# Kernel tuning notes

Hardware: AMD Instinct MI355X
Metric: run time of the kernel (lower is better)

## Reference

```python
import jax, jax.numpy as jnp
import numpy as np

D_MODEL = 1024
NHEAD = 16
D_K = D_MODEL // NHEAD  # 64
B, L = 2, 2048


def _apply_rotary(x, cos, sin):
    # x: (B, H, L, d_k); cos/sin: (B, L, d_k//2)
    d_half = x.shape[-1] // 2
    x1, x2 = x[..., :d_half], x[..., d_half:]
    c = cos[:, None, :, :]
    s = sin[:, None, :, :]
    return jnp.concatenate([x1 * c - x2 * s, x1 * s + x2 * c], axis=-1)


def setup_inputs() -> dict:
    key = jax.random.key(0)
    ks = jax.random.split(key, 7)
    x = jax.random.normal(ks[0], (B, L, D_MODEL), dtype=jnp.float32)
    rope_cos = jax.random.uniform(ks[1], (B, L, D_K // 2), dtype=jnp.float32)
    rope_sin = jax.random.uniform(ks[2], (B, L, D_K // 2), dtype=jnp.float32)
    # Linear params (PyTorch layout: weight (out, in), y = x @ W.T + b)
    lim_qkv = 1.0 / np.sqrt(D_MODEL)
    W_qkv = jax.random.uniform(ks[3], (3 * D_MODEL, D_MODEL), dtype=jnp.float32, minval=-lim_qkv, maxval=lim_qkv)
    b_qkv = jax.random.uniform(ks[4], (3 * D_MODEL,), dtype=jnp.float32, minval=-lim_qkv, maxval=lim_qkv)
    W_out = jax.random.uniform(ks[5], (D_MODEL, D_MODEL), dtype=jnp.float32, minval=-lim_qkv, maxval=lim_qkv)
    b_out = jax.random.uniform(ks[6], (D_MODEL,), dtype=jnp.float32, minval=-lim_qkv, maxval=lim_qkv)
    return {"x": x, "rope_cos": rope_cos, "rope_sin": rope_sin,
            "W_qkv": W_qkv, "b_qkv": b_qkv, "W_out": W_out, "b_out": b_out}


def reference(x, rope_cos, rope_sin, W_qkv, b_qkv, W_out, b_out):
    Bx, Lx, D = x.shape
    scale = D_K ** -0.5
    qkv = x @ W_qkv.T + b_qkv                     # (B, L, 3D)
    qkv = qkv.reshape(Bx, Lx, 3, NHEAD, D_K)
    q = jnp.transpose(qkv[:, :, 0], (0, 2, 1, 3))  # (B, H, L, d_k)
    k = jnp.transpose(qkv[:, :, 1], (0, 2, 1, 3))
    v = jnp.transpose(qkv[:, :, 2], (0, 2, 1, 3))
    q = _apply_rotary(q, rope_cos, rope_sin)
    k = _apply_rotary(k, rope_cos, rope_sin)
    attn = jnp.einsum("bhqd,bhkd->bhqk", q, k) * scale  # (B, H, L, L)
    attn = jax.nn.softmax(attn, axis=-1)
    out = jnp.einsum("bhqk,bhkd->bhqd", attn, v)          # (B, H, L, d_k)
    out = jnp.transpose(out, (0, 2, 1, 3)).reshape(Bx, Lx, D)
    return out @ W_out.T + b_out
```

## Files before the change

kernel.cpp:

```cpp
#include <hip/hip_runtime.h>
#include <hip/hip_bf16.h>
#include <stdint.h>


typedef __attribute__((ext_vector_type(8)))  short bf16x8;
typedef __attribute__((ext_vector_type(4)))  float f32x4;
typedef __attribute__((ext_vector_type(16))) float f32x16;
typedef __attribute__((ext_vector_type(4)))  short short4v;
typedef __attribute__((ext_vector_type(4)))  unsigned int u32x4;

#define DEV static __device__ __forceinline__

DEV short f2bf(float f) {
  uint32_t u = __builtin_bit_cast(uint32_t, f);
  u += 0x7FFFu + ((u >> 16) & 1u);
  return (short)(u >> 16);
}
DEV float bf2f(short s) {
  return __builtin_bit_cast(float, ((uint32_t)(uint16_t)s) << 16);
}
DEV uint32_t pkbf(float a, float b) {
  __hip_bfloat162 h = __float22bfloat162_rn(make_float2(a, b));
  uint32_t u;
  __builtin_memcpy(&u, &h, 4);
  return u;
}
DEV void pl32swap(uint32_t &dst, uint32_t &src) {
  asm volatile("v_permlane32_swap_b32 %0, %1" : "+v"(dst), "+v"(src));
}

#define AS1 __attribute__((address_space(1)))
#define AS3 __attribute__((address_space(3)))
#define GLOAD_LDS16(gp, lp) \
  __builtin_amdgcn_global_load_lds((const AS1 void*)(gp), (AS3 void*)(lp), 16, 0, 0)

__global__ void k_cvt_bf16(const float* __restrict__ in, short* __restrict__ out, int n4) {
  int i = blockIdx.x * 256 + threadIdx.x;
  if (i >= n4) return;
  float4 v = reinterpret_cast<const float4*>(in)[i];
  short4v o = { f2bf(v.x), f2bf(v.y), f2bf(v.z), f2bf(v.w) };
  reinterpret_cast<short4v*>(out)[i] = o;
}

DEV void gemm_stage(const short* Ag, const short* Bg, int K_,
                    short* AsD, short* BsD, int tid) {
  #pragma unroll
  for (int p = 0; p < 4; ++p) {
    int f = p * 256 + tid;
    int row = f >> 3;
    int sch = (f & 7) ^ (row & 7);
    GLOAD_LDS16(Ag + (size_t)row * K_ + sch * 8, AsD + f * 8);
    GLOAD_LDS16(Bg + (size_t)row * K_ + sch * 8, BsD + f * 8);
  }
}

#define GEMM_BODY(A_, Bt_, K_)                                              \
  __shared__ short Lds[4 * 128 * 64];    \
  const int tid = threadIdx.x;                                              \
  const int lane = tid & 63;                                                \
  const int wid  = tid >> 6;                                                \
  const int lq = lane & 15, lg = lane >> 4;                                 \
  const int wr = wid >> 1, wc = wid & 1;                                    \
  const int m0 = blockIdx.y * 128;                                          \
  const int n0 = blockIdx.x * 128;                                          \
  f32x4 acc[4][4];                                                          \
  _Pragma("unroll")                                                         \
  for (int i = 0; i < 4; ++i)                                               \
    _Pragma("unroll")                                                       \
    for (int j = 0; j < 4; ++j) acc[i][j] = (f32x4){0.f, 0.f, 0.f, 0.f};    \
  const int KT = (K_) >> 6;                                                 \
  gemm_stage((A_) + (size_t)m0 * (K_), (Bt_) + (size_t)n0 * (K_), (K_),     \
             Lds, Lds + 8192, tid);                                         \
  __syncthreads();                                                          \
  int gbuf = 0;                                                             \
  for (int kt = 0; kt < KT; ++kt) {                                         \
    if (kt + 1 < KT)                                                        \
      gemm_stage((A_)  + (size_t)m0 * (K_) + (kt + 1) * 64,                 \
                 (Bt_) + (size_t)n0 * (K_) + (kt + 1) * 64, (K_),           \
                 Lds + (gbuf ^ 1) * 16384,                                  \
                 Lds + (gbuf ^ 1) * 16384 + 8192, tid);                     \
    const short* As = Lds + gbuf * 16384;                                   \
    const short* Bs = As + 8192;                                            \
    _Pragma("unroll")                                                       \
    for (int kk = 0; kk < 2; ++kk) {                                        \
      bf16x8 af[4], bfr[4];                                                 \
      _Pragma("unroll")                                                     \
      for (int i = 0; i < 4; ++i)                                           \
        af[i]  = *reinterpret_cast<const bf16x8*>(                          \
            &As[(wr*64 + i*16 + lq) * 64 + (((kk*4 + lg) ^ (lq & 7)) * 8)]);\
      _Pragma("unroll")                                                     \
      for (int j = 0; j < 4; ++j)                                           \
        bfr[j] = *reinterpret_cast<const bf16x8*>(                          \
            &Bs[(wc*64 + j*16 + lq) * 64 + (((kk*4 + lg) ^ (lq & 7)) * 8)]);\
      _Pragma("unroll")                                                     \
      for (int i = 0; i < 4; ++i)                                           \
        _Pragma("unroll")                                                   \
        for (int j = 0; j < 4; ++j)                                         \
          acc[i][j] = __builtin_amdgcn_mfma_f32_16x16x32_bf16(              \
              af[i], bfr[j], acc[i][j], 0, 0, 0);                           \
    }                                                                       \
    __syncthreads();                                                        \
    gbuf ^= 1;                                                              \
  }

__global__ __launch_bounds__(256) void k_gemm_qkv(
    const short* __restrict__ A, const short* __restrict__ Bt,
    const float* __restrict__ bias,
    const float* __restrict__ cosb, const float* __restrict__ sinb,
    short* __restrict__ Qb, short* __restrict__ Kb, short* __restrict__ Vt)
{
  GEMM_BODY(A, Bt, 1024)

  short* Ep = Lds + wid * 4096;
  const int cglob = n0 + wc * 64;
  if (cglob < 2048) {
    const bool isq = (cglob < 1024);
    const float QS = isq ? 0.125f * 1.4426950408889634f : 1.0f;
    short* dst = isq ? Qb : Kb;
    const int h = (cglob & 1023) >> 6;
    const float b0 = bias[cglob + lq],      b2 = bias[cglob + 32 + lq];
    const float b1 = bias[cglob + 16 + lq], b3 = bias[cglob + 48 + lq];
    #pragma unroll
    for (int i = 0; i < 4; ++i) {
      #pragma unroll
      for (int r = 0; r < 4; ++r) {
        int lloc = i*16 + lg*4 + r;
        int rg = m0 + wr*64 + lloc;
        float c0 = cosb[(size_t)rg * 32 + lq];
        float s0 = sinb[(size_t)rg * 32 + lq];
        float c1 = cosb[(size_t)rg * 32 + 16 + lq];
        float s1 = sinb[(size_t)rg * 32 + 16 + lq];
        float x1 = acc[i][0][r] + b0, x2 = acc[i][2][r] + b2;
        Ep[lloc*64 + lq]      = f2bf((x1 * c0 - x2 * s0) * QS);
        Ep[lloc*64 + 32 + lq] = f2bf((x1 * s0 + x2 * c0) * QS);
        float y1 = acc[i][1][r] + b1, y2 = acc[i][3][r] + b3;
        Ep[lloc*64 + 16 + lq] = f2bf((y1 * c1 - y2 * s1) * QS);
        Ep[lloc*64 + 48 + lq] = f2bf((y1 * s1 + y2 * c1) * QS);
      }
    }
    #pragma unroll
    for (int p = 0; p < 8; ++p) {
      int f = p * 64 + lane;
      int lloc = f >> 3, d0 = (f & 7) * 8;
      int rg = m0 + wr*64 + lloc;
      int bi = rg >> 11, ll = rg & 2047;
      bf16x8 v = *reinterpret_cast<const bf16x8*>(&Ep[lloc*64 + d0]);
      *reinterpret_cast<bf16x8*>(
          &dst[((size_t)(bi * 16 + h) * 2048 + ll) * 64 + d0]) = v;
    }
  } else {
    const int h = (cglob - 2048) >> 6;
    #pragma unroll
    for (int i = 0; i < 4; ++i) {
      int lloc = i*16 + lg*4;
      #pragma unroll
      for (int j = 0; j < 4; ++j) {
        int d = j * 16 + lq;
        float bv = bias[cglob + d];
        short4v pk4 = { f2bf(acc[i][j][0] + bv), f2bf(acc[i][j][1] + bv),
                        f2bf(acc[i][j][2] + bv), f2bf(acc[i][j][3] + bv) };
        *reinterpret_cast<short4v*>(
            &Ep[d*64 + (lloc ^ ((d & 7) << 3))]) = pk4;
      }
    }
    #pragma unroll
    for (int p = 0; p < 8; ++p) {
      int f = p * 64 + lane;
      int d = f >> 3, lc = (f & 7) * 8;
      bf16x8 v = *reinterpret_cast<const bf16x8*>(&Ep[d*64 + lc]);
      int lreal = lc ^ ((d & 7) << 3);
      int rg = m0 + wr*64 + lreal;
      int bi = rg >> 11, ll = rg & 2047;
      *reinterpret_cast<bf16x8*>(
          &Vt[((size_t)(bi * 16 + h) * 64 + d) * 2048 + ll]) = v;
    }
  }
}

__global__ __launch_bounds__(256) void k_gemm_out(
    const short* __restrict__ A, const short* __restrict__ Bt,
    const float* __restrict__ bias, float* __restrict__ C)
{
  GEMM_BODY(A, Bt, 1024)
  const int N = 1024;
  #pragma unroll
  for (int i = 0; i < 4; ++i) {
    int rbase = m0 + wr*64 + i*16 + lg*4;
    #pragma unroll
    for (int j = 0; j < 4; ++j) {
      int col = n0 + wc*64 + j*16 + lq;
      float bv = bias[col];
      #pragma unroll
      for (int r = 0; r < 4; ++r)
        C[(size_t)(rbase + r) * N + col] = acc[i][j][r] + bv;
    }
  }
}

__global__ __launch_bounds__(256, 4) void k_attn(
    const short* __restrict__ Q, const short* __restrict__ Kb,
    const short* __restrict__ Vt,
    short* __restrict__ P0, short* __restrict__ P1,
    float* __restrict__ L0, float* __restrict__ L1)
{
  __shared__ short Ks[2][64 * 64];
  __shared__ short Vs[2][64 * 64];
  const int tid = threadIdx.x;
  const int lane = tid & 63;
  const int wid  = tid >> 6;
  const int Lq = lane & 31;
  const int h  = lane >> 5;
  const int bh = blockIdx.y;
  const int q0 = blockIdx.x * 128 + wid * 32;
  const int b = bh >> 4, hh = bh & 15;
  const int t0 = blockIdx.z * 16;
  short* Pp = blockIdx.z ? P1 : P0;
  float* Lp = blockIdx.z ? L1 : L0;

  const short* Qp = Q  + ((size_t)bh * 2048 + q0 + Lq) * 64;
  const short* Kp = Kb + (size_t)bh * 2048 * 64;
  const short* Vp = Vt + (size_t)bh * 64 * 2048;

  #define STAGE_KV(c, t) do {                                              \
    const short* Kg_ = Kp + (size_t)(t) * 64 * 64;                         \
    const short* Vg_ = Vp + (size_t)(t) * 64;                              \
    _Pragma("unroll")                                                      \
    for (int p_ = 0; p_ < 2; ++p_) {                                       \
      int f_ = p_ * 256 + tid;                                             \
      int row_ = f_ >> 3;                                                  \
      int sch_ = (f_ & 7) ^ (row_ & 7);                                    \
      GLOAD_LDS16(Kg_ + row_ * 64 + sch_ * 8,            &Ks[c][f_ * 8]);  \
      GLOAD_LDS16(Vg_ + (size_t)row_ * 2048 + sch_ * 8,  &Vs[c][f_ * 8]);  \
    }                                                                      \
  } while (0)

  bf16x8 qf[4];
  #pragma unroll
  for (int ks = 0; ks < 4; ++ks)
    qf[ks] = *reinterpret_cast<const bf16x8*>(Qp + ks * 16 + h * 8);

  f32x16 o[2];
  #pragma unroll
  for (int nd = 0; nd < 2; ++nd)
    #pragma unroll
    for (int r = 0; r < 16; ++r) o[nd][r] = 0.f;
  float la0 = 0.f, la1 = 0.f;

  STAGE_KV(0, t0);
  asm volatile("s_waitcnt vmcnt(0)" ::: "memory");
  __syncthreads();

  for (int kk2 = 0; kk2 < 16; ++kk2) {
    const int cur = kk2 & 1;
    if (kk2 < 15) STAGE_KV(cur ^ 1, t0 + kk2 + 1);

    #pragma unroll
    for (int mb = 0; mb < 2; ++mb) {
      f32x16 sm;
      #pragma unroll
      for (int r = 0; r < 16; ++r) sm[r] = 0.f;
      #pragma unroll
      for (int ks = 0; ks < 4; ++ks) {
        bf16x8 kf = *reinterpret_cast<const bf16x8*>(
            &Ks[cur][(mb*32 + Lq) * 64 + (((ks*2 + h) ^ (Lq & 7)) * 8)]);
        sm = __builtin_amdgcn_mfma_f32_32x32x16_bf16(kf, qf[ks], sm, 0, 0, 0);
      }
      #pragma unroll
      for (int half = 0; half < 2; ++half) {
        float e0 = __builtin_amdgcn_exp2f(sm[8*half + 0]);
        float e1 = __builtin_amdgcn_exp2f(sm[8*half + 1]);
        float e2 = __builtin_amdgcn_exp2f(sm[8*half + 2]);
        float e3 = __builtin_amdgcn_exp2f(sm[8*half + 3]);
        float e4 = __builtin_amdgcn_exp2f(sm[8*half + 4]);
        float e5 = __builtin_amdgcn_exp2f(sm[8*half + 5]);
        float e6 = __builtin_amdgcn_exp2f(sm[8*half + 6]);
        float e7 = __builtin_amdgcn_exp2f(sm[8*half + 7]);
        la0 += (e0 + e1) + (e4 + e5);
        la1 += (e2 + e3) + (e6 + e7);
        uint32_t w0 = pkbf(e0, e1), w1 = pkbf(e2, e3);
        uint32_t w2 = pkbf(e4, e5), w3 = pkbf(e6, e7);
        pl32swap(w0, w2);
        pl32swap(w1, w3);
        u32x4 paw = { w0, w1, w2, w3 };
        bf16x8 pa = __builtin_bit_cast(bf16x8, paw);
        const int ksl = mb * 2 + half;
        #pragma unroll
        for (int nd = 0; nd < 2; ++nd) {
          bf16x8 vf = *reinterpret_cast<const bf16x8*>(
              &Vs[cur][(nd*32 + Lq) * 64 + (((ksl*2 + h) ^ (Lq & 7)) * 8)]);
          o[nd] = __builtin_amdgcn_mfma_f32_32x32x16_bf16(pa, vf, o[nd], 0, 0, 0);
        }
      }
    }
    asm volatile("s_waitcnt vmcnt(0)" ::: "memory");
    __syncthreads();
  }

  float l_part = la0 + la1;
  l_part += __shfl_xor(l_part, 32, 64);
  if (h == 0) Lp[((size_t)bh << 11) + q0 + Lq] = l_part;
  #pragma unroll
  for (int r = 0; r < 16; ++r) {
    int qrow = (r & 3) + 8 * (r >> 2) + 4 * h;
    size_t rowb = ((size_t)b * 2048 + q0 + qrow) * 1024 + hh * 64;
    Pp[rowb + Lq]      = f2bf(o[0][r]);
    Pp[rowb + 32 + Lq] = f2bf(o[1][r]);
  }
  #undef STAGE_KV
}

__global__ void k_merge(const short* __restrict__ P0, const short* __restrict__ P1,
                        const float* __restrict__ L0, const float* __restrict__ L1,
                        short* __restrict__ AO)
{
  int idx = blockIdx.x * 256 + threadIdx.x;
  int rg = idx >> 7;
  int c0 = (idx & 127) * 8;
  int bh = ((rg >> 11) << 4) + (c0 >> 6);
  size_t lix = ((size_t)bh << 11) + (rg & 2047);
  float inv = 1.f / (L0[lix] + L1[lix]);
  size_t off = (size_t)rg * 1024 + c0;
  bf16x8 a = *reinterpret_cast<const bf16x8*>(&P0[off]);
  bf16x8 bv = *reinterpret_cast<const bf16x8*>(&P1[off]);
  bf16x8 r;
  #pragma unroll
  for (int j = 0; j < 8; ++j)
    r[j] = f2bf((bf2f(a[j]) + bf2f(bv[j])) * inv);
  *reinterpret_cast<bf16x8*>(&AO[off]) = r;
}

extern "C" void kernel_launch(void* const* d_in, const int* in_sizes, int n_in,
                              void* d_out, int out_size, void* d_ws, size_t ws_size,
                              hipStream_t stream) {
  (void)in_sizes; (void)n_in; (void)out_size; (void)ws_size;
  const float* x    = (const float*)d_in[0];
  const float* rc   = (const float*)d_in[1];
  const float* rs   = (const float*)d_in[2];
  const float* Wqkv = (const float*)d_in[3];
  const float* bqkv = (const float*)d_in[4];
  const float* Wout = (const float*)d_in[5];
  const float* bout = (const float*)d_in[6];
  float* out = (float*)d_out;

  char* ws = (char*)d_ws;
  short* xb  = (short*)(ws);
  short* wqb = (short*)(ws + 8388608);
  short* wob = (short*)(ws + 14680064);
  short* Qb  = (short*)(ws + 16777216);
  short* Kb  = (short*)(ws + 25165824);
  short* Vt  = (short*)(ws + 33554432);
  short* P0  = (short*)(ws + 41943040);
  short* P1  = (short*)(ws + 50331648);
  float* L0  = (float*)(ws + 58720256);
  float* L1  = (float*)(ws + 58982400);

  k_cvt_bf16<<<4096, 256, 0, stream>>>(x,    xb,  1048576);
  k_cvt_bf16<<<3072, 256, 0, stream>>>(Wqkv, wqb, 786432);
  k_cvt_bf16<<<1024, 256, 0, stream>>>(Wout, wob, 262144);
  k_gemm_qkv<<<dim3(24, 32), 256, 0, stream>>>(xb, wqb, bqkv, rc, rs, Qb, Kb, Vt);
  k_attn<<<dim3(16, 32, 2), 256, 0, stream>>>(Qb, Kb, Vt, P0, P1, L0, L1);
  k_merge<<<2048, 256, 0, stream>>>(P0, P1, L0, L1, P0);
  k_gemm_out<<<dim3(8, 32), 256, 0, stream>>>(P0, wob, bout, out);
}
```

Before: 120.0 us.

## Fuse split-KV merge into output GEMM, remap blocks across XCDs, prioritize MFMA

Removes the separate merge kernel. The output projection GEMM now loads both partial attention outputs and their softmax denominators itself, normalises them in registers and writes the A tile into LDS, while the weight tile keeps using direct global-to-LDS loads. This drops one launch and one round trip through HBM for the merged activation, but adds register-staged loads and a division per element to the GEMM's main loop. It also remaps block IDs in the GEMMs and attention so neighbouring tiles land on the same XCD for L2 reuse, and raises wave priority around the MFMA sections in attention.

Measured after the change: 128.4 us. +7.1%, slower.

```diff
diff --git a/kernel.cpp b/kernel.cpp
--- a/kernel.cpp
+++ b/kernel.cpp
@@ -61,8 +61,11 @@
   const int wid  = tid >> 6;                                                \
   const int lq = lane & 15, lg = lane >> 4;                                 \
   const int wr = wid >> 1, wc = wid & 1;                                    \
-  const int m0 = blockIdx.y * 128;                                          \
-  const int n0 = blockIdx.x * 128;                                          \
+  int lin_ = blockIdx.y * gridDim.x + blockIdx.x;                           \
+  const int q_ = (gridDim.x * gridDim.y) >> 3;                              \
+  lin_ = (lin_ & 7) * q_ + (lin_ >> 3);                                     \
+  const int m0 = (lin_ / gridDim.x) * 128;                                  \
+  const int n0 = (lin_ % gridDim.x) * 128;                                  \
   f32x4 acc[4][4];                                                          \
   _Pragma("unroll")                                                         \
   for (int i = 0; i < 4; ++i)                                               \
@@ -178,10 +181,109 @@
 }
 
 __global__ __launch_bounds__(256) void k_gemm_out(
-    const short* __restrict__ A, const short* __restrict__ Bt,
+    const short* __restrict__ P0, const short* __restrict__ P1,
+    const float* __restrict__ L0, const float* __restrict__ L1,
+    const short* __restrict__ Bt,
     const float* __restrict__ bias, float* __restrict__ C)
 {
-  GEMM_BODY(A, Bt, 1024)
+  __shared__ short Lds[4 * 128 * 64];
+  const int tid = threadIdx.x;
+  const int lane = tid & 63;
+  const int wid  = tid >> 6;
+  const int lq = lane & 15, lg = lane >> 4;
+  const int wr = wid >> 1, wc = wid & 1;
+  int lin = blockIdx.y * gridDim.x + blockIdx.x;
+  lin = (lin & 7) * 32 + (lin >> 3);
+  const int m0 = (lin >> 3) * 128;
+  const int n0 = (lin & 7) * 128;
+
+  f32x4 acc[4][4];
+  #pragma unroll
+  for (int i = 0; i < 4; ++i)
+    #pragma unroll
+    for (int j = 0; j < 4; ++j) acc[i][j] = (f32x4){0.f, 0.f, 0.f, 0.f};
+
+  bf16x8 pa_[4], pb_[4];
+  float  ll0_[4], ll1_[4];
+
+  #define AO_LOAD(kt) do {                                                 \
+    _Pragma("unroll")                                                      \
+    for (int c = 0; c < 4; ++c) {                                          \
+      int f = c * 256 + tid;                                               \
+      int row = f >> 3;                                                    \
+      int rg = m0 + row;                                                   \
+      int sch = (f & 7) ^ (row & 7);                                       \
+      size_t off = (size_t)rg * 1024 + (size_t)(kt) * 64 + sch * 8;        \
+      pa_[c] = *reinterpret_cast<const bf16x8*>(&P0[off]);                 \
+      pb_[c] = *reinterpret_cast<const bf16x8*>(&P1[off]);                 \
+      size_t lix = ((size_t)((rg >> 11) * 16 + (kt)) << 11) + (rg & 2047); \
+      ll0_[c] = L0[lix]; ll1_[c] = L1[lix];                                \
+    }                                                                      \
+  } while (0)
+  #define AO_WRITE(slot) do {                                              \
+    _Pragma("unroll")                                                      \
+    for (int c = 0; c < 4; ++c) {                                          \
+      int f = c * 256 + tid;                                               \
+      float inv = 1.f / (ll0_[c] + ll1_[c]);                               \
+      uint32_t w0_ = pkbf((bf2f(pa_[c][0]) + bf2f(pb_[c][0])) * inv,       \
+                          (bf2f(pa_[c][1]) + bf2f(pb_[c][1])) * inv);      \
+      uint32_t w1_ = pkbf((bf2f(pa_[c][2]) + bf2f(pb_[c][2])) * inv,       \
+                          (bf2f(pa_[c][3]) + bf2f(pb_[c][3])) * inv);      \
+      uint32_t w2_ = pkbf((bf2f(pa_[c][4]) + bf2f(pb_[c][4])) * inv,       \
+                          (bf2f(pa_[c][5]) + bf2f(pb_[c][5])) * inv);      \
+      uint32_t w3_ = pkbf((bf2f(pa_[c][6]) + bf2f(pb_[c][6])) * inv,       \
+                          (bf2f(pa_[c][7]) + bf2f(pb_[c][7])) * inv);      \
+      u32x4 wv = { w0_, w1_, w2_, w3_ };                                   \
+      *reinterpret_cast<u32x4*>(&Lds[(slot) * 16384 + f * 8]) = wv;        \
+    }                                                                      \
+  } while (0)
+  #define BO_STAGE(slot, kt) do {                                         \
+    const short* Bg = Bt + (size_t)n0 * 1024 + (kt) * 64;                  \
+    _Pragma("unroll")                                                      \
+    for (int p = 0; p < 4; ++p) {                                          \
+      int f = p * 256 + tid;                                               \
+      int row = f >> 3;                                                    \
+      int sch = (f & 7) ^ (row & 7);                                       \
+      GLOAD_LDS16(Bg + (size_t)row * 1024 + sch * 8,                       \
+                  Lds + (slot) * 16384 + 8192 + f * 8);                    \
+    }                                                                      \
+  } while (0)
+
+  AO_LOAD(0);
+  BO_STAGE(0, 0);
+  AO_WRITE(0);
+  __syncthreads();
+
+  for (int kt = 0; kt < 16; ++kt) {
+    const int slot = kt & 1;
+    if (kt < 15) {
+      AO_LOAD(kt + 1);
+      BO_STAGE(slot ^ 1, kt + 1);
+    }
+    const short* As = Lds + slot * 16384;
+    const short* Bs = As + 8192;
+    #pragma unroll
+    for (int kk = 0; kk < 2; ++kk) {
+      bf16x8 af[4], bfr[4];
+      #pragma unroll
+      for (int i = 0; i < 4; ++i)
+        af[i]  = *reinterpret_cast<const bf16x8*>(
+            &As[(wr*64 + i*16 + lq) * 64 + (((kk*4 + lg) ^ (lq & 7)) * 8)]);
+      #pragma unroll
+      for (int j = 0; j < 4; ++j)
+        bfr[j] = *reinterpret_cast<const bf16x8*>(
+            &Bs[(wc*64 + j*16 + lq) * 64 + (((kk*4 + lg) ^ (lq & 7)) * 8)]);
+      #pragma unroll
+      for (int i = 0; i < 4; ++i)
+        #pragma unroll
+        for (int j = 0; j < 4; ++j)
+          acc[i][j] = __builtin_amdgcn_mfma_f32_16x16x32_bf16(
+              af[i], bfr[j], acc[i][j], 0, 0, 0);
+    }
+    if (kt < 15) AO_WRITE(slot ^ 1);
+    __syncthreads();
+  }
+
   const int N = 1024;
   #pragma unroll
   for (int i = 0; i < 4; ++i) {
@@ -195,6 +297,9 @@
         C[(size_t)(rbase + r) * N + col] = acc[i][j][r] + bv;
     }
   }
+  #undef AO_LOAD
+  #undef AO_WRITE
+  #undef BO_STAGE
 }
 
 __global__ __launch_bounds__(256, 4) void k_attn(
@@ -210,12 +315,16 @@
   const int wid  = tid >> 6;
   const int Lq = lane & 31;
   const int h  = lane >> 5;
-  const int bh = blockIdx.y;
-  const int q0 = blockIdx.x * 128 + wid * 32;
+  int lin = (blockIdx.z * gridDim.y + blockIdx.y) * gridDim.x + blockIdx.x;
+  lin = (lin & 7) * 128 + (lin >> 3);
+  const int bx = lin & 15;
+  const int bh = (lin >> 4) & 31;
+  const int bz = lin >> 9;
+  const int q0 = bx * 128 + wid * 32;
   const int b = bh >> 4, hh = bh & 15;
-  const int t0 = blockIdx.z * 16;
-  short* Pp = blockIdx.z ? P1 : P0;
-  float* Lp = blockIdx.z ? L1 : L0;
+  const int t0 = bz * 16;
+  short* Pp = bz ? P1 : P0;
+  float* Lp = bz ? L1 : L0;
 
   const short* Qp = Q  + ((size_t)bh * 2048 + q0 + Lq) * 64;
   const short* Kp = Kb + (size_t)bh * 2048 * 64;
@@ -259,12 +368,14 @@
       f32x16 sm;
       #pragma unroll
       for (int r = 0; r < 16; ++r) sm[r] = 0.f;
+      __builtin_amdgcn_s_setprio(1);
       #pragma unroll
       for (int ks = 0; ks < 4; ++ks) {
         bf16x8 kf = *reinterpret_cast<const bf16x8*>(
             &Ks[cur][(mb*32 + Lq) * 64 + (((ks*2 + h) ^ (Lq & 7)) * 8)]);
         sm = __builtin_amdgcn_mfma_f32_32x32x16_bf16(kf, qf[ks], sm, 0, 0, 0);
       }
+      __builtin_amdgcn_s_setprio(0);
       #pragma unroll
       for (int half = 0; half < 2; ++half) {
         float e0 = __builtin_amdgcn_exp2f(sm[8*half + 0]);
@@ -284,12 +395,14 @@
         u32x4 paw = { w0, w1, w2, w3 };
         bf16x8 pa = __builtin_bit_cast(bf16x8, paw);
         const int ksl = mb * 2 + half;
+        __builtin_amdgcn_s_setprio(1);
         #pragma unroll
         for (int nd = 0; nd < 2; ++nd) {
           bf16x8 vf = *reinterpret_cast<const bf16x8*>(
               &Vs[cur][(nd*32 + Lq) * 64 + (((ksl*2 + h) ^ (Lq & 7)) * 8)]);
           o[nd] = __builtin_amdgcn_mfma_f32_32x32x16_bf16(pa, vf, o[nd], 0, 0, 0);
         }
+        __builtin_amdgcn_s_setprio(0);
       }
     }
     asm volatile("s_waitcnt vmcnt(0)" ::: "memory");
@@ -307,26 +420,6 @@
     Pp[rowb + 32 + Lq] = f2bf(o[1][r]);
   }
   #undef STAGE_KV
-}
-
-__global__ void k_merge(const short* __restrict__ P0, const short* __restrict__ P1,
-                        const float* __restrict__ L0, const float* __restrict__ L1,
-                        short* __restrict__ AO)
-{
-  int idx = blockIdx.x * 256 + threadIdx.x;
-  int rg = idx >> 7;
-  int c0 = (idx & 127) * 8;
-  int bh = ((rg >> 11) << 4) + (c0 >> 6);
-  size_t lix = ((size_t)bh << 11) + (rg & 2047);
-  float inv = 1.f / (L0[lix] + L1[lix]);
-  size_t off = (size_t)rg * 1024 + c0;
-  bf16x8 a = *reinterpret_cast<const bf16x8*>(&P0[off]);
-  bf16x8 bv = *reinterpret_cast<const bf16x8*>(&P1[off]);
-  bf16x8 r;
-  #pragma unroll
-  for (int j = 0; j < 8; ++j)
-    r[j] = f2bf((bf2f(a[j]) + bf2f(bv[j])) * inv);
-  *reinterpret_cast<bf16x8*>(&AO[off]) = r;
 }
 
 extern "C" void kernel_launch(void* const* d_in, const int* in_sizes, int n_in,
@@ -359,6 +452,5 @@
   k_cvt_bf16<<<1024, 256, 0, stream>>>(Wout, wob, 262144);
   k_gemm_qkv<<<dim3(24, 32), 256, 0, stream>>>(xb, wqb, bqkv, rc, rs, Qb, Kb, Vt);
   k_attn<<<dim3(16, 32, 2), 256, 0, stream>>>(Qb, Kb, Vt, P0, P1, L0, L1);
-  k_merge<<<2048, 256, 0, stream>>>(P0, P1, L0, L1, P0);
-  k_gemm_out<<<dim3(8, 32), 256, 0, stream>>>(P0, wob, bout, out);
-}
+  k_gemm_out<<<dim3(8, 32), 256, 0, stream>>>(P0, P1, L0, L1, wob, bout, out);
+}
```
